# Optimization experiments

Measured on AMD Instinct MI355X. Metric: run time of the kernel, lower is better.

Reference implementation:

```python
import jax, jax.numpy as jnp
import numpy as np
from jax import lax

GAMMA = 0.01   # SoftDTWLossPyTorch(gamma=0.01)
INF = 1e10     # large finite sentinel for out-of-band DP cells (safe exp underflow)
C1 = 0.01 ** 2 # piqa SSIM constants, value_range=1
C2 = 0.03 ** 2


def _gauss_kernel(size=11, sigma=1.5):
    g = np.exp(-0.5 * ((np.arange(size) - (size - 1) / 2.0) / sigma) ** 2)
    g = g / g.sum()
    return jnp.asarray(np.outer(g, g).astype(np.float32))


def _blur(x, k2d):
    # depthwise valid Gaussian filter; x: [P, C, H, W]
    P, C, H, W = x.shape
    y = lax.conv_general_dilated(x.reshape(P * C, 1, H, W), k2d[None, None], (1, 1), 'VALID')
    return y.reshape(P, C, y.shape[-2], y.shape[-1])


def _ssim_pairs(x, y):
    # x, y: [P, 3, H, W] in [0,1]; returns per-pair mean SSIM [P] (piqa SSIM, reduction='none')
    k2d = _gauss_kernel()
    mu_x = _blur(x, k2d)
    mu_y = _blur(y, k2d)
    sxx = _blur(x * x, k2d) - mu_x ** 2
    syy = _blur(y * y, k2d) - mu_y ** 2
    sxy = _blur(x * y, k2d) - mu_x * mu_y
    num = (2.0 * mu_x * mu_y + C1) * (2.0 * sxy + C2)
    den = (mu_x ** 2 + mu_y ** 2 + C1) * (sxx + syy + C2)
    return (num / den).mean(axis=(1, 2, 3))


def _soft_dtw(x, y, gamma=GAMMA):
    # squared-euclidean soft-DTW for every (b, s) pair, wavefront over anti-diagonals
    # x: [B, T], y: [S, T] -> [B, S]
    B, T = x.shape
    S = y.shape[0]
    D = (x[:, None, :, None] - y[None, :, None, :]) ** 2  # [B, S, T, T]
    ii = jnp.arange(T)
    kk = jnp.arange(2 * T - 1)
    jj = kk[:, None] - ii[None, :]              # column index of cell i on diag k
    valid = (jj >= 0) & (jj < T)                # [2T-1, T]
    Dd = jnp.moveaxis(D[:, :, ii[None, :], jnp.clip(jj, 0, T - 1)], 2, 0)  # [2T-1, B, S, T]
    i0 = ii == 0

    def softmin3(a, b, c):
        m = jnp.minimum(jnp.minimum(a, b), c)
        return m - gamma * jnp.log(
            jnp.exp(-(a - m) / gamma) + jnp.exp(-(b - m) / gamma) + jnp.exp(-(c - m) / gamma))

    def step(carry, xs):
        r2, r1 = carry                     # diagonals k-2, k-1, each [B, S, T]
        d, v, k = xs
        pad = jnp.full(r1.shape[:-1] + (1,), INF, r1.dtype)
        r1s = jnp.concatenate([pad, r1[..., :-1]], axis=-1)  # R[i-1, j]
        r2s = jnp.concatenate([pad, r2[..., :-1]], axis=-1)  # R[i-1, j-1]
        sm = softmin3(r2s, r1s, r1)        # r1 itself is R[i, j-1]
        sm = jnp.where((k == 0) & i0, 0.0, sm)  # base cell R[0,0] = D[0,0]
        r = jnp.where(v, d + sm, INF)
        return (r1, r), None

    init = (jnp.full((B, S, T), INF, jnp.float32), jnp.full((B, S, T), INF, jnp.float32))
    (_, rf), _ = lax.scan(step, init, (Dd, valid, kk))
    return rf[..., -1]  # R[T-1, T-1]


def _forward(input, samples, img, sample_img, output, labels):
    B = input.shape[0]
    S = samples.shape[0]
    # all (sample, batch-image) pairs for SSIM; ssim(sample_img[i], img[b])
    X = jnp.broadcast_to(sample_img[None], (B,) + sample_img.shape).reshape((B * S,) + sample_img.shape[1:])
    Y = jnp.broadcast_to(img[:, None], (B, S) + img.shape[1:]).reshape((B * S,) + img.shape[1:])
    ssim = _ssim_pairs(X, Y).reshape(B, S)
    m0 = (1.0 - ssim) * 10.0
    m1 = _soft_dtw(input, samples) / 500.0
    per_b = ((m0 + m1) / 2.0).mean(axis=1)   # metrics.mean(dim=2).mean(dim=1)
    metric_sum = per_b.sum()
    # torch BCELoss with log clamped at -100
    ln = jnp.clip(jnp.log(output), -100.0, None)
    ln1 = jnp.clip(jnp.log1p(-output), -100.0, None)
    bce = -jnp.mean(labels * ln + (1.0 - labels) * ln1)
    loss = bce + metric_sum / 10.0
    return loss, bce, metric_sum


def setup_inputs() -> dict:
    key = jax.random.key(0)
    k1, k2, k3, k4, k5, k6 = jax.random.split(key, 6)
    B, S, T, H, W = 32, 8, 256, 128, 128
    return {
        'input': jax.random.normal(k1, (B, T), dtype=jnp.float32),
        'samples': jax.random.normal(k2, (S, T), dtype=jnp.float32),
        'img': jax.random.uniform(k3, (B, 3, H, W), dtype=jnp.float32),
        'sample_img': jax.random.uniform(k4, (S, 3, H, W), dtype=jnp.float32),
        'output': jax.random.uniform(k5, (B, 1), dtype=jnp.float32) * 0.98 + 0.01,
        'labels': (jax.random.uniform(k6, (B, 1)) < 0.5).astype(jnp.float32),
    }


def reference(input, samples, img, sample_img, output, labels):
    return _forward(input, samples, img, sample_img, output, labels)
```

## Files before the change

### kernel.cpp

```cpp
#include <hip/hip_runtime.h>
#include <math.h>

#define IW 128
#define OW 118
#define OWP 120
#define NPIX (IW*IW)
#define MOW (OW*OW)
#define NS 8
#define NB 32
#define NIMG 40
#define TT 256
#define SC1 0.0001f
#define SC2 0.0009f
#define NBAND 4
#define BROWS 30

__device__ __forceinline__ unsigned bfp(float x) {
    unsigned u = __float_as_uint(x);
    return (u + 0x7fffu + ((u >> 16) & 1u)) >> 16;
}
__device__ __forceinline__ float bflo(unsigned w) { return __uint_as_float(w << 16); }
__device__ __forceinline__ float bfhi(unsigned w) { return __uint_as_float(w & 0xffff0000u); }

__device__ __forceinline__ void gauss_regs(float* g) {
    float s = 0.f;
#pragma unroll
    for (int i = 0; i < 11; ++i) { float t = (i - 5) * (1.0f / 1.5f); g[i] = expf(-0.5f * t * t); s += g[i]; }
    float inv = 1.f / s;
#pragma unroll
    for (int i = 0; i < 11; ++i) g[i] *= inv;
}

__global__ __launch_bounds__(256) void k_mom(const float* __restrict__ img,
        const float* __restrict__ simg, unsigned* __restrict__ MOM) {
    __shared__ float sR[NIMG * IW + 8];
    __shared__ float sHv[NIMG * OWP];
    __shared__ float sHs[NIMG * OWP];
    int cb = blockIdx.x, im = blockIdx.y;
    int ch = cb >> 2, band = cb & 3;
    int r0 = band * BROWS;
    int nrows = (118 - r0 < BROWS) ? (118 - r0) : BROWS;
    int in_rows = nrows + 10;
    const float* src = (im < NS) ? (simg + (size_t)(im * 3 + ch) * NPIX)
                                 : (img  + (size_t)((im - NS) * 3 + ch) * NPIX);
    float g[11]; gauss_regs(g);
    int t = threadIdx.x;
    for (int i4 = t; i4 < in_rows * (IW / 4); i4 += 256) {
        int r = i4 >> 5, c4 = i4 & 31;
        ((float4*)sR)[(r << 5) + c4] = ((const float4*)(src + (size_t)(r0 + r) * IW))[c4];
    }
    __syncthreads();
    {
        int cg = t & 31, tr = t >> 5;
        for (int rb = 0; rb < in_rows; rb += 8) {
            int r = rb + tr;
            if (r < in_rows && cg < 30) {
                const float* p = sR + r * IW + cg * 4;
                float4 A = *(const float4*)p, B = *(const float4*)(p + 4), C = *(const float4*)(p + 8);
                float2 D = *(const float2*)(p + 12);
                float w[14] = {A.x,A.y,A.z,A.w,B.x,B.y,B.z,B.w,C.x,C.y,C.z,C.w,D.x,D.y};
                float a0=0,a1=0,a2=0,a3=0,q0=0,q1=0,q2=0,q3=0;
#pragma unroll
                for (int k = 0; k < 11; ++k) {
                    float gk = g[k];
                    a0=fmaf(gk,w[k],a0); a1=fmaf(gk,w[k+1],a1); a2=fmaf(gk,w[k+2],a2); a3=fmaf(gk,w[k+3],a3);
                    q0=fmaf(gk,w[k]*w[k],q0); q1=fmaf(gk,w[k+1]*w[k+1],q1);
                    q2=fmaf(gk,w[k+2]*w[k+2],q2); q3=fmaf(gk,w[k+3]*w[k+3],q3);
                }
                *(float4*)(sHv + r * OWP + cg * 4) = make_float4(a0,a1,a2,a3);
                *(float4*)(sHs + r * OWP + cg * 4) = make_float4(q0,q1,q2,q3);
            }
        }
    }
    __syncthreads();
    unsigned* out = MOM + (size_t)(im * 3 + ch) * MOW;
    int c = t & 127, rg = t >> 7;
    if (c < 118) {
        for (int r = rg; r < nrows; r += 2) {
            float a = 0.f, q = 0.f;
#pragma unroll
            for (int k = 0; k < 11; ++k) {
                float gk = g[k];
                int ro = (r + k) * OWP + c;
                a = fmaf(gk, sHv[ro], a);
                q = fmaf(gk, sHs[ro], q);
            }
            float var = q - a * a;
            out[(size_t)(r0 + r) * OW + c] = bfp(a) | (bfp(var) << 16);
        }
    }
}

__global__ __launch_bounds__(256) void k_pairdtw(const float* __restrict__ img,
        const float* __restrict__ simg, const unsigned* __restrict__ MOM,
        float* __restrict__ SP, const float* __restrict__ input,
        const float* __restrict__ samples, float* __restrict__ dtw) {
    __shared__ float SM[NIMG * IW + 8 + NIMG * OWP];
    int bid = blockIdx.x;
    int t = threadIdx.x;
    if (bid < 64) {
        const float FINF = 1e10f;
        int w = t >> 6, l = t & 63;
        int pair = bid * 4 + w;
        int b = pair >> 3, s = pair & 7;
        float* sY = SM + (w << 8);
        *(float4*)(sY + l * 4) = *(const float4*)(samples + s * TT + l * 4);
        float4 xv = *(const float4*)(input + b * TT + l * 4);
        float x0 = xv.x, x1 = xv.y, x2 = xv.z, x3 = xv.w;
        __syncthreads();
        float left0 = FINF, left1 = FINF, left2 = FINF, left3 = FINF;
        float bot0 = FINF, bot1 = FINF, bot1p = FINF;
        for (int m = 0; m < 191; ++m) {
            float t0  = __shfl_up(bot0, 1);
            float t1  = __shfl_up(bot1, 1);
            float tdl = __shfl_up(bot1p, 1);
            if (l == 0) { t0 = FINF; t1 = FINF; tdl = FINF; }
            int c = m - l;
            if (0 <= c && c < 128) {
                float2 yv = *(const float2*)(sY + 2 * c);
                float y0 = yv.x, y1 = yv.y;
                bot1p = bot1;
                float up0 = t0, up1 = t1, dg = tdl, v0, v1;
#define CELLH(x_, y_, a_, b_, c_, out_) { float d_ = (x_) - (y_); \
                out_ = fmaf(d_, d_, fminf(fminf((a_), (b_)), (c_))); }
                CELLH(x0, y0, dg, up0, left0, v0);
                if ((l | c) == 0) { float d0 = x0 - y0; v0 = d0 * d0; }
                CELLH(x0, y1, up0, up1, v0, v1);
                dg = left0; left0 = v1; up0 = v0; up1 = v1;
                CELLH(x1, y0, dg, up0, left1, v0);
                CELLH(x1, y1, up0, up1, v0, v1);
                dg = left1; left1 = v1; up0 = v0; up1 = v1;
                CELLH(x2, y0, dg, up0, left2, v0);
                CELLH(x2, y1, up0, up1, v0, v1);
                dg = left2; left2 = v1; up0 = v0; up1 = v1;
                CELLH(x3, y0, dg, up0, left3, v0);
                CELLH(x3, y1, up0, up1, v0, v1);
                left3 = v1; up0 = v0; up1 = v1;
                bot0 = up0; bot1 = up1;
            }
        }
        if (l == 63) dtw[pair] = bot1;
        return;
    }
    int pid = bid - 64;
    int xcd = pid & 7;
    int idx = pid >> 3;
    int q = (idx >= 288) ? 3 : (idx >= 192) ? 2 : (idx >= 96) ? 1 : 0;
    int rem = idx - q * 96;
    int b = xcd * 4 + q;
    int s = rem & 7;
    int cb = rem >> 3;
    int ch = cb >> 2, band = cb & 3;
    int r0 = band * BROWS;
    int nrows = (118 - r0 < BROWS) ? (118 - r0) : BROWS;
    int in_rows = nrows + 10;
    float* sP = SM;
    float* sH = SM + NIMG * IW + 8;
    const float* xs = simg + (size_t)(s * 3 + ch) * NPIX;
    const float* ys = img  + (size_t)(b * 3 + ch) * NPIX;
    float g[11]; gauss_regs(g);
    for (int i4 = t; i4 < in_rows * (IW / 4); i4 += 256) {
        int r = i4 >> 5, c4 = i4 & 31;
        float4 xv = ((const float4*)(xs + (size_t)(r0 + r) * IW))[c4];
        float4 yv = ((const float4*)(ys + (size_t)(r0 + r) * IW))[c4];
        ((float4*)sP)[(r << 5) + c4] = make_float4(xv.x*yv.x, xv.y*yv.y, xv.z*yv.z, xv.w*yv.w);
    }
    __syncthreads();
    {
        int cg = t & 31, tr = t >> 5;
        for (int rb = 0; rb < in_rows; rb += 8) {
            int r = rb + tr;
            if (r < in_rows && cg < 30) {
                const float* p = sP + r * IW + cg * 4;
                float4 A = *(const float4*)p, B = *(const float4*)(p + 4), C = *(const float4*)(p + 8);
                float2 D = *(const float2*)(p + 12);
                float w[14] = {A.x,A.y,A.z,A.w,B.x,B.y,B.z,B.w,C.x,C.y,C.z,C.w,D.x,D.y};
                float o0=0,o1=0,o2=0,o3=0;
#pragma unroll
                for (int k = 0; k < 11; ++k) {
                    float gk = g[k];
                    o0=fmaf(gk,w[k],o0); o1=fmaf(gk,w[k+1],o1); o2=fmaf(gk,w[k+2],o2); o3=fmaf(gk,w[k+3],o3);
                }
                *(float4*)(sH + r * OWP + cg * 4) = make_float4(o0,o1,o2,o3);
            }
        }
    }
    __syncthreads();
    const unsigned* Mx = MOM + (size_t)(s * 3 + ch) * MOW;
    const unsigned* My = MOM + (size_t)((NS + b) * 3 + ch) * MOW;
    float lsum = 0.f;
    int c = t & 127, rg = t >> 7;
    if (c < 118) {
        for (int r = rg; r < nrows; r += 2) {
            float bxy = 0.f;
#pragma unroll
            for (int k = 0; k < 11; ++k) bxy = fmaf(g[k], sH[(r + k) * OWP + c], bxy);
            size_t gidx = (size_t)(r0 + r) * OW + c;
            unsigned wx = Mx[gidx], wy = My[gidx];
            float ux = bflo(wx), sxx = bfhi(wx);
            float uy = bflo(wy), syy = bfhi(wy);
            float sxy = bxy - ux * uy;
            float num = (2.f * ux * uy + SC1) * (2.f * sxy + SC2);
            float den = (ux * ux + uy * uy + SC1) * (sxx + syy + SC2);
            lsum += num * __builtin_amdgcn_rcpf(den);
        }
    }
#pragma unroll
    for (int off = 32; off > 0; off >>= 1) lsum += __shfl_down(lsum, off);
    if ((t & 63) == 0) sP[t >> 6] = lsum;
    __syncthreads();
    int pair = b * 8 + s;
    if (t == 0) SP[((pair * 3) + ch) * NBAND + band] = sP[0] + sP[1] + sP[2] + sP[3];
}

__global__ __launch_bounds__(256) void k_final(const float* __restrict__ SP,
        const float* __restrict__ DTW, const float* __restrict__ outp,
        const float* __restrict__ lab, float* __restrict__ out) {
    __shared__ float redm[4], redb[4];
    int t = threadIdx.x;
    float ssum = 0.f;
#pragma unroll
    for (int i = 0; i < 3 * NBAND; ++i) ssum += SP[t * 3 * NBAND + i];
    float ssim = ssum * (1.0f / 41772.0f);
    float m0 = (1.f - ssim) * 10.f;
    float m1 = DTW[t] * (1.f / 500.f);
    float m = (m0 + m1) * 0.5f;
    float bt = 0.f;
    if (t < 32) {
        float o = outp[t], l = lab[t];
        float ln  = fmaxf(logf(o), -100.f);
        float ln1 = fmaxf(log1pf(-o), -100.f);
        bt = l * ln + (1.f - l) * ln1;
    }
#pragma unroll
    for (int off = 32; off > 0; off >>= 1) { m += __shfl_down(m, off); bt += __shfl_down(bt, off); }
    if ((t & 63) == 0) { redm[t >> 6] = m; redb[t >> 6] = bt; }
    __syncthreads();
    if (t == 0) {
        float msum = redm[0] + redm[1] + redm[2] + redm[3];
        float bsum = redb[0] + redb[1] + redb[2] + redb[3];
        float metric_sum = msum * 0.125f;
        float bce = -bsum * (1.f / 32.f);
        out[0] = bce + metric_sum * 0.1f;
        out[1] = bce;
        out[2] = metric_sum;
    }
}

extern "C" void kernel_launch(void* const* d_in, const int* in_sizes, int n_in,
                              void* d_out, int out_size, void* d_ws, size_t ws_size,
                              hipStream_t stream) {
    const float* input   = (const float*)d_in[0];
    const float* samples = (const float*)d_in[1];
    const float* img     = (const float*)d_in[2];
    const float* simg    = (const float*)d_in[3];
    const float* outp    = (const float*)d_in[4];
    const float* lab     = (const float*)d_in[5];
    float* out = (float*)d_out;
    unsigned* MOM = (unsigned*)d_ws;
    float* SP  = (float*)d_ws + (size_t)NIMG * 3 * MOW;
    float* DTW = SP + 256 * 3 * NBAND;

    k_mom    <<<dim3(12, 40),    dim3(256), 0, stream>>>(img, simg, MOM);
    k_pairdtw<<<dim3(64 + 3072), dim3(256), 0, stream>>>(img, simg, MOM, SP, input, samples, DTW);
    k_final  <<<dim3(1),         dim3(256), 0, stream>>>(SP, DTW, outp, lab, out);
}
```

Baseline: 114.2 us.

## Fuse final reduction via last-block atomic counter; register-blocked vertical blur

Removes the separate k_final launch: every block of k_pairdtw increments an atomic counter (reset in k_mom), and the last block to finish performs the final SSIM/DTW/BCE reduction. The vertical Gaussian pass in both k_mom and the pair kernel is restructured so each thread computes 15 consecutive output rows from 25 shared-memory loads held in register accumulators, instead of 11 loads per output row. This trades one launch and redundant LDS reads for more registers per thread and an extra atomic per block.

```diff
diff --git a/kernel.cpp b/kernel.cpp
--- a/kernel.cpp
+++ b/kernel.cpp
@@ -14,6 +14,8 @@
 #define SC2 0.0009f
 #define NBAND 4
 #define BROWS 30
+#define NPAIRBLK 3072
+#define NBLK_TOTAL (64 + NPAIRBLK)
 
 __device__ __forceinline__ unsigned bfp(float x) {
     unsigned u = __float_as_uint(x);
@@ -31,12 +33,19 @@
     for (int i = 0; i < 11; ++i) g[i] *= inv;
 }
 
+#define CELLH(x_, y_, a_, b_, c_, out_) { float d_ = (x_) - (y_); \
+    out_ = fmaf(d_, d_, fminf(fminf((a_), (b_)), (c_))); }
+
 __global__ __launch_bounds__(256) void k_mom(const float* __restrict__ img,
-        const float* __restrict__ simg, unsigned* __restrict__ MOM) {
+        const float* __restrict__ simg, unsigned* __restrict__ MOM,
+        unsigned* __restrict__ cnt) {
     __shared__ float sR[NIMG * IW + 8];
     __shared__ float sHv[NIMG * OWP];
     __shared__ float sHs[NIMG * OWP];
     int cb = blockIdx.x, im = blockIdx.y;
+    int t = threadIdx.x;
+    if (cb == 0 && im == 0 && t == 0)
+        __hip_atomic_store(cnt, 0u, __ATOMIC_RELAXED, __HIP_MEMORY_SCOPE_AGENT);
     int ch = cb >> 2, band = cb & 3;
     int r0 = band * BROWS;
     int nrows = (118 - r0 < BROWS) ? (118 - r0) : BROWS;
@@ -44,7 +53,6 @@
     const float* src = (im < NS) ? (simg + (size_t)(im * 3 + ch) * NPIX)
                                  : (img  + (size_t)((im - NS) * 3 + ch) * NPIX);
     float g[11]; gauss_regs(g);
-    int t = threadIdx.x;
     for (int i4 = t; i4 < in_rows * (IW / 4); i4 += 256) {
         int r = i4 >> 5, c4 = i4 & 31;
         ((float4*)sR)[(r << 5) + c4] = ((const float4*)(src + (size_t)(r0 + r) * IW))[c4];
@@ -75,27 +83,40 @@
     __syncthreads();
     unsigned* out = MOM + (size_t)(im * 3 + ch) * MOW;
     int c = t & 127, rg = t >> 7;
+    int base = rg * 15;
+    int nout = nrows - base; if (nout > 15) nout = 15;
     if (c < 118) {
-        for (int r = rg; r < nrows; r += 2) {
-            float a = 0.f, q = 0.f;
-#pragma unroll
-            for (int k = 0; k < 11; ++k) {
-                float gk = g[k];
-                int ro = (r + k) * OWP + c;
-                a = fmaf(gk, sHv[ro], a);
-                q = fmaf(gk, sHs[ro], q);
-            }
-            float var = q - a * a;
-            out[(size_t)(r0 + r) * OW + c] = bfp(a) | (bfp(var) << 16);
-        }
+        float av[15], aq[15];
+#pragma unroll
+        for (int i = 0; i < 15; ++i) { av[i] = 0.f; aq[i] = 0.f; }
+#pragma unroll
+        for (int j = 0; j < 25; ++j) {
+            float hv = sHv[(base + j) * OWP + c];
+            float hq = sHs[(base + j) * OWP + c];
+#pragma unroll
+            for (int o = 0; o < 15; ++o)
+                if (o >= j - 10 && o <= j) {
+                    av[o] = fmaf(g[j - o], hv, av[o]);
+                    aq[o] = fmaf(g[j - o], hq, aq[o]);
+                }
+        }
+#pragma unroll
+        for (int o = 0; o < 15; ++o)
+            if (o < nout) {
+                float m = av[o], var = aq[o] - m * m;
+                out[(size_t)(r0 + base + o) * OW + c] = bfp(m) | (bfp(var) << 16);
+            }
     }
 }
 
 __global__ __launch_bounds__(256) void k_pairdtw(const float* __restrict__ img,
         const float* __restrict__ simg, const unsigned* __restrict__ MOM,
         float* __restrict__ SP, const float* __restrict__ input,
-        const float* __restrict__ samples, float* __restrict__ dtw) {
+        const float* __restrict__ samples, float* __restrict__ dtw,
+        unsigned* __restrict__ cnt, const float* __restrict__ outp,
+        const float* __restrict__ lab, float* __restrict__ out) {
     __shared__ float SM[NIMG * IW + 8 + NIMG * OWP];
+    __shared__ unsigned slast;
     int bid = blockIdx.x;
     int t = threadIdx.x;
     if (bid < 64) {
@@ -121,8 +142,6 @@
                 float y0 = yv.x, y1 = yv.y;
                 bot1p = bot1;
                 float up0 = t0, up1 = t1, dg = tdl, v0, v1;
-#define CELLH(x_, y_, a_, b_, c_, out_) { float d_ = (x_) - (y_); \
-                out_ = fmaf(d_, d_, fminf(fminf((a_), (b_)), (c_))); }
                 CELLH(x0, y0, dg, up0, left0, v0);
                 if ((l | c) == 0) { float d0 = x0 - y0; v0 = d0 * d0; }
                 CELLH(x0, y1, up0, up1, v0, v1);
@@ -139,111 +158,130 @@
                 bot0 = up0; bot1 = up1;
             }
         }
-        if (l == 63) dtw[pair] = bot1;
-        return;
-    }
-    int pid = bid - 64;
-    int xcd = pid & 7;
-    int idx = pid >> 3;
-    int q = (idx >= 288) ? 3 : (idx >= 192) ? 2 : (idx >= 96) ? 1 : 0;
-    int rem = idx - q * 96;
-    int b = xcd * 4 + q;
-    int s = rem & 7;
-    int cb = rem >> 3;
-    int ch = cb >> 2, band = cb & 3;
-    int r0 = band * BROWS;
-    int nrows = (118 - r0 < BROWS) ? (118 - r0) : BROWS;
-    int in_rows = nrows + 10;
-    float* sP = SM;
-    float* sH = SM + NIMG * IW + 8;
-    const float* xs = simg + (size_t)(s * 3 + ch) * NPIX;
-    const float* ys = img  + (size_t)(b * 3 + ch) * NPIX;
-    float g[11]; gauss_regs(g);
-    for (int i4 = t; i4 < in_rows * (IW / 4); i4 += 256) {
-        int r = i4 >> 5, c4 = i4 & 31;
-        float4 xv = ((const float4*)(xs + (size_t)(r0 + r) * IW))[c4];
-        float4 yv = ((const float4*)(ys + (size_t)(r0 + r) * IW))[c4];
-        ((float4*)sP)[(r << 5) + c4] = make_float4(xv.x*yv.x, xv.y*yv.y, xv.z*yv.z, xv.w*yv.w);
-    }
-    __syncthreads();
-    {
-        int cg = t & 31, tr = t >> 5;
-        for (int rb = 0; rb < in_rows; rb += 8) {
-            int r = rb + tr;
-            if (r < in_rows && cg < 30) {
-                const float* p = sP + r * IW + cg * 4;
-                float4 A = *(const float4*)p, B = *(const float4*)(p + 4), C = *(const float4*)(p + 8);
-                float2 D = *(const float2*)(p + 12);
-                float w[14] = {A.x,A.y,A.z,A.w,B.x,B.y,B.z,B.w,C.x,C.y,C.z,C.w,D.x,D.y};
-                float o0=0,o1=0,o2=0,o3=0;
-#pragma unroll
-                for (int k = 0; k < 11; ++k) {
-                    float gk = g[k];
-                    o0=fmaf(gk,w[k],o0); o1=fmaf(gk,w[k+1],o1); o2=fmaf(gk,w[k+2],o2); o3=fmaf(gk,w[k+3],o3);
+        if (l == 63)
+            __hip_atomic_store(&dtw[pair], bot1, __ATOMIC_RELAXED, __HIP_MEMORY_SCOPE_AGENT);
+    } else {
+        int pid = bid - 64;
+        int xcd = pid & 7;
+        int idx = pid >> 3;
+        int q = (idx >= 288) ? 3 : (idx >= 192) ? 2 : (idx >= 96) ? 1 : 0;
+        int rem = idx - q * 96;
+        int b = xcd * 4 + q;
+        int s = rem & 7;
+        int cb = rem >> 3;
+        int ch = cb >> 2, band = cb & 3;
+        int r0 = band * BROWS;
+        int nrows = (118 - r0 < BROWS) ? (118 - r0) : BROWS;
+        int in_rows = nrows + 10;
+        float* sP = SM;
+        float* sH = SM + NIMG * IW + 8;
+        const float* xs = simg + (size_t)(s * 3 + ch) * NPIX;
+        const float* ys = img  + (size_t)(b * 3 + ch) * NPIX;
+        float g[11]; gauss_regs(g);
+        for (int i4 = t; i4 < in_rows * (IW / 4); i4 += 256) {
+            int r = i4 >> 5, c4 = i4 & 31;
+            float4 xv = ((const float4*)(xs + (size_t)(r0 + r) * IW))[c4];
+            float4 yv = ((const float4*)(ys + (size_t)(r0 + r) * IW))[c4];
+            ((float4*)sP)[(r << 5) + c4] = make_float4(xv.x*yv.x, xv.y*yv.y, xv.z*yv.z, xv.w*yv.w);
+        }
+        __syncthreads();
+        {
+            int cg = t & 31, tr = t >> 5;
+            for (int rb = 0; rb < in_rows; rb += 8) {
+                int r = rb + tr;
+                if (r < in_rows && cg < 30) {
+                    const float* p = sP + r * IW + cg * 4;
+                    float4 A = *(const float4*)p, B = *(const float4*)(p + 4), C = *(const float4*)(p + 8);
+                    float2 D = *(const float2*)(p + 12);
+                    float w[14] = {A.x,A.y,A.z,A.w,B.x,B.y,B.z,B.w,C.x,C.y,C.z,C.w,D.x,D.y};
+                    float o0=0,o1=0,o2=0,o3=0;
+#pragma unroll
+                    for (int k = 0; k < 11; ++k) {
+                        float gk = g[k];
+                        o0=fmaf(gk,w[k],o0); o1=fmaf(gk,w[k+1],o1); o2=fmaf(gk,w[k+2],o2); o3=fmaf(gk,w[k+3],o3);
+                    }
+                    *(float4*)(sH + r * OWP + cg * 4) = make_float4(o0,o1,o2,o3);
                 }
-                *(float4*)(sH + r * OWP + cg * 4) = make_float4(o0,o1,o2,o3);
-            }
-        }
-    }
-    __syncthreads();
-    const unsigned* Mx = MOM + (size_t)(s * 3 + ch) * MOW;
-    const unsigned* My = MOM + (size_t)((NS + b) * 3 + ch) * MOW;
-    float lsum = 0.f;
-    int c = t & 127, rg = t >> 7;
-    if (c < 118) {
-        for (int r = rg; r < nrows; r += 2) {
-            float bxy = 0.f;
-#pragma unroll
-            for (int k = 0; k < 11; ++k) bxy = fmaf(g[k], sH[(r + k) * OWP + c], bxy);
-            size_t gidx = (size_t)(r0 + r) * OW + c;
-            unsigned wx = Mx[gidx], wy = My[gidx];
-            float ux = bflo(wx), sxx = bfhi(wx);
-            float uy = bflo(wy), syy = bfhi(wy);
-            float sxy = bxy - ux * uy;
-            float num = (2.f * ux * uy + SC1) * (2.f * sxy + SC2);
-            float den = (ux * ux + uy * uy + SC1) * (sxx + syy + SC2);
-            lsum += num * __builtin_amdgcn_rcpf(den);
-        }
-    }
-#pragma unroll
-    for (int off = 32; off > 0; off >>= 1) lsum += __shfl_down(lsum, off);
-    if ((t & 63) == 0) sP[t >> 6] = lsum;
-    __syncthreads();
-    int pair = b * 8 + s;
-    if (t == 0) SP[((pair * 3) + ch) * NBAND + band] = sP[0] + sP[1] + sP[2] + sP[3];
-}
-
-__global__ __launch_bounds__(256) void k_final(const float* __restrict__ SP,
-        const float* __restrict__ DTW, const float* __restrict__ outp,
-        const float* __restrict__ lab, float* __restrict__ out) {
-    __shared__ float redm[4], redb[4];
-    int t = threadIdx.x;
-    float ssum = 0.f;
-#pragma unroll
-    for (int i = 0; i < 3 * NBAND; ++i) ssum += SP[t * 3 * NBAND + i];
-    float ssim = ssum * (1.0f / 41772.0f);
-    float m0 = (1.f - ssim) * 10.f;
-    float m1 = DTW[t] * (1.f / 500.f);
-    float m = (m0 + m1) * 0.5f;
-    float bt = 0.f;
-    if (t < 32) {
-        float o = outp[t], l = lab[t];
-        float ln  = fmaxf(logf(o), -100.f);
-        float ln1 = fmaxf(log1pf(-o), -100.f);
-        bt = l * ln + (1.f - l) * ln1;
-    }
-#pragma unroll
-    for (int off = 32; off > 0; off >>= 1) { m += __shfl_down(m, off); bt += __shfl_down(bt, off); }
-    if ((t & 63) == 0) { redm[t >> 6] = m; redb[t >> 6] = bt; }
+            }
+        }
+        __syncthreads();
+        const unsigned* Mx = MOM + (size_t)(s * 3 + ch) * MOW;
+        const unsigned* My = MOM + (size_t)((NS + b) * 3 + ch) * MOW;
+        float lsum = 0.f;
+        int c = t & 127, rg = t >> 7;
+        int base = rg * 15;
+        int nout = nrows - base; if (nout > 15) nout = 15;
+        if (c < 118) {
+            float acc[15];
+#pragma unroll
+            for (int i = 0; i < 15; ++i) acc[i] = 0.f;
+#pragma unroll
+            for (int j = 0; j < 25; ++j) {
+                float h = sH[(base + j) * OWP + c];
+#pragma unroll
+                for (int o = 0; o < 15; ++o)
+                    if (o >= j - 10 && o <= j)
+                        acc[o] = fmaf(g[j - o], h, acc[o]);
+            }
+#pragma unroll
+            for (int o = 0; o < 15; ++o)
+                if (o < nout) {
+                    size_t gidx = (size_t)(r0 + base + o) * OW + c;
+                    unsigned wx = Mx[gidx], wy = My[gidx];
+                    float ux = bflo(wx), sxx = bfhi(wx);
+                    float uy = bflo(wy), syy = bfhi(wy);
+                    float sxy = acc[o] - ux * uy;
+                    float num = (2.f * ux * uy + SC1) * (2.f * sxy + SC2);
+                    float den = (ux * ux + uy * uy + SC1) * (sxx + syy + SC2);
+                    lsum += num * __builtin_amdgcn_rcpf(den);
+                }
+        }
+#pragma unroll
+        for (int off = 32; off > 0; off >>= 1) lsum += __shfl_down(lsum, off);
+        if ((t & 63) == 0) sP[t >> 6] = lsum;
+        __syncthreads();
+        if (t == 0) {
+            int pair = b * 8 + s;
+            __hip_atomic_store(&SP[((pair * 3) + ch) * NBAND + band],
+                               sP[0] + sP[1] + sP[2] + sP[3],
+                               __ATOMIC_RELAXED, __HIP_MEMORY_SCOPE_AGENT);
+        }
+    }
     __syncthreads();
     if (t == 0) {
-        float msum = redm[0] + redm[1] + redm[2] + redm[3];
-        float bsum = redb[0] + redb[1] + redb[2] + redb[3];
-        float metric_sum = msum * 0.125f;
-        float bce = -bsum * (1.f / 32.f);
-        out[0] = bce + metric_sum * 0.1f;
-        out[1] = bce;
-        out[2] = metric_sum;
+        unsigned old = __hip_atomic_fetch_add(cnt, 1u, __ATOMIC_ACQ_REL, __HIP_MEMORY_SCOPE_AGENT);
+        slast = (old == NBLK_TOTAL - 1) ? 1u : 0u;
+    }
+    __syncthreads();
+    if (slast) {
+        float m = 0.f, bt = 0.f;
+        if (t < 32) {
+            float ssum = 0.f;
+            const float* SPb = SP + t * 96;
+#pragma unroll
+            for (int i = 0; i < 96; ++i)
+                ssum += __hip_atomic_load(&SPb[i], __ATOMIC_RELAXED, __HIP_MEMORY_SCOPE_AGENT);
+            float dsum = 0.f;
+#pragma unroll
+            for (int s2 = 0; s2 < 8; ++s2)
+                dsum += __hip_atomic_load(&dtw[t * 8 + s2], __ATOMIC_RELAXED, __HIP_MEMORY_SCOPE_AGENT);
+            m = (80.f - ssum * (10.f / 41772.f) + dsum * (1.f / 500.f)) * (1.f / 16.f);
+            float o = outp[t], l = lab[t];
+            float ln  = fmaxf(logf(o), -100.f);
+            float ln1 = fmaxf(log1pf(-o), -100.f);
+            bt = l * ln + (1.f - l) * ln1;
+        }
+        if (t < 64) {
+#pragma unroll
+            for (int off = 32; off > 0; off >>= 1) { m += __shfl_down(m, off); bt += __shfl_down(bt, off); }
+            if (t == 0) {
+                float metric_sum = m;
+                float bce = -bt * (1.f / 32.f);
+                out[0] = bce + metric_sum * 0.1f;
+                out[1] = bce;
+                out[2] = metric_sum;
+            }
+        }
     }
 }
 
@@ -260,8 +298,9 @@
     unsigned* MOM = (unsigned*)d_ws;
     float* SP  = (float*)d_ws + (size_t)NIMG * 3 * MOW;
     float* DTW = SP + 256 * 3 * NBAND;
-
-    k_mom    <<<dim3(12, 40),    dim3(256), 0, stream>>>(img, simg, MOM);
-    k_pairdtw<<<dim3(64 + 3072), dim3(256), 0, stream>>>(img, simg, MOM, SP, input, samples, DTW);
-    k_final  <<<dim3(1),         dim3(256), 0, stream>>>(SP, DTW, outp, lab, out);
-}
+    unsigned* cnt = (unsigned*)(DTW + 256);
+
+    k_mom    <<<dim3(12, 40),        dim3(256), 0, stream>>>(img, simg, MOM, cnt);
+    k_pairdtw<<<dim3(NBLK_TOTAL),    dim3(256), 0, stream>>>(img, simg, MOM, SP, input, samples,
+                                                             DTW, cnt, outp, lab, out);
+}
```

Measured after the change: 169.5 us. 1.48x slower.
